# Optimization experiments

Measured on AMD Instinct MI355X. Metric: run time of the kernel, lower is better.

## Reference

```python
import jax, jax.numpy as jnp
import numpy as np
import math

D = 64  # block size == head dim


def _sdpa(q, k, v):
    # q,k,v: [..., n, d]
    d = q.shape[-1]
    scores = jnp.einsum('...nd,...md->...nm', q / math.sqrt(d), k)
    probs = jax.nn.softmax(scores, axis=-1)
    return jnp.einsum('...nm,...md->...nd', probs, v)


def setup_inputs() -> dict:
    key = jax.random.key(0)
    kq, kk, kv = jax.random.split(key, 3)
    B, H, N = 4, 16, 4128  # N = 64*64 + 32 -> nonzero remainder
    q = jax.random.normal(kq, (B, H, N, D), dtype=jnp.float32)
    k = jax.random.normal(kk, (B, H, N, D), dtype=jnp.float32)
    v = jax.random.normal(kv, (B, H, N, D), dtype=jnp.float32)
    return {'q': q, 'k': k, 'v': v}


def reference(q, k, v):
    B, H, N, d = q.shape
    ND = d * (N // d)          # length covered by full DxD blocks
    h = H * (ND // d)          # total number of block-heads
    Q = q[:, :, :ND, :].reshape(B, h, d, d)
    K = k[:, :, :ND, :].reshape(B, h, d, d)
    V = v[:, :, :ND, :].reshape(B, h, d, d)
    attn_main = _sdpa(Q, K, V).reshape(B, H, ND, d)
    attn_rem = _sdpa(q[:, :, ND:, :], k[:, :, ND:, :], v[:, :, ND:, :])
    return jnp.concatenate([attn_main, attn_rem], axis=-2)
```

## Files before the change

kernel.cpp:

```cpp
#include <hip/hip_runtime.h>
#include <math.h>

#define STR 65

__global__ __launch_bounds__(256, 3) void bda_kernel(
    const float* __restrict__ qg,
    const float* __restrict__ kg,
    const float* __restrict__ vg,
    float* __restrict__ og,
    int N, int nblk, int rem) {
  __shared__ float Qs[64 * STR];
  __shared__ float Ks[64 * STR];
  __shared__ float Vs[64 * STR];

  const int wg  = blockIdx.x;
  const int blk = wg % nblk;
  const int bh  = wg / nblk;
  const int nrows = (blk == nblk - 1 && rem != 0) ? rem : 64;
  const size_t base = ((size_t)bh * (size_t)N + (size_t)blk * 64) * 64;

  const int t = threadIdx.x;

#pragma unroll
  for (int i = 0; i < 4; ++i) {
    const int e   = (t << 2) + (i << 10);
    const int row = e >> 6;
    const int col = e & 63;
    float4 qv = make_float4(0.f, 0.f, 0.f, 0.f);
    float4 kv = qv, vv = qv;
    if (row < nrows) {
      qv = *(const float4*)(qg + base + e);
      kv = *(const float4*)(kg + base + e);
      vv = *(const float4*)(vg + base + e);
    }
    const int a = row * STR + col;
    Qs[a + 0] = qv.x; Qs[a + 1] = qv.y; Qs[a + 2] = qv.z; Qs[a + 3] = qv.w;
    Ks[a + 0] = kv.x; Ks[a + 1] = kv.y; Ks[a + 2] = kv.z; Ks[a + 3] = kv.w;
    Vs[a + 0] = vv.x; Vs[a + 1] = vv.y; Vs[a + 2] = vv.z; Vs[a + 3] = vv.w;
  }
  __syncthreads();

  const int tx = t & 15;
  const int ty = t >> 4;
  const int r0 = ty << 2;
  const int c0 = tx << 2;

  float acc[4][4] = {{0.f}};
  {
    const float* q0 = &Qs[(r0 + 0) * STR];
    const float* q1 = &Qs[(r0 + 1) * STR];
    const float* q2 = &Qs[(r0 + 2) * STR];
    const float* q3 = &Qs[(r0 + 3) * STR];
    const float* k0 = &Ks[(c0 + 0) * STR];
    const float* k1 = &Ks[(c0 + 1) * STR];
    const float* k2 = &Ks[(c0 + 2) * STR];
    const float* k3 = &Ks[(c0 + 3) * STR];
#pragma unroll 4
    for (int kk = 0; kk < 64; ++kk) {
      const float a0 = q0[kk], a1 = q1[kk], a2 = q2[kk], a3 = q3[kk];
      const float b0 = k0[kk], b1 = k1[kk], b2 = k2[kk], b3 = k3[kk];
      acc[0][0] += a0 * b0; acc[0][1] += a0 * b1; acc[0][2] += a0 * b2; acc[0][3] += a0 * b3;
      acc[1][0] += a1 * b0; acc[1][1] += a1 * b1; acc[1][2] += a1 * b2; acc[1][3] += a1 * b3;
      acc[2][0] += a2 * b0; acc[2][1] += a2 * b1; acc[2][2] += a2 * b2; acc[2][3] += a2 * b3;
      acc[3][0] += a3 * b0; acc[3][1] += a3 * b1; acc[3][2] += a3 * b2; acc[3][3] += a3 * b3;
    }
  }
  __syncthreads();
#pragma unroll
  for (int i = 0; i < 4; ++i)
#pragma unroll
    for (int j = 0; j < 4; ++j)
      Qs[(r0 + i) * STR + c0 + j] = acc[i][j] * 0.125f;
  __syncthreads();

  {
    const int r = t >> 2;
    const int p = t & 3;
    float s[16];
    float m = -INFINITY;
#pragma unroll
    for (int c = 0; c < 16; ++c) {
      const int col = (p << 4) + c;
      const float x = Qs[r * STR + col];
      s[c] = x;
      m = (col < nrows) ? fmaxf(m, x) : m;
    }
    m = fmaxf(m, __shfl_xor(m, 1));
    m = fmaxf(m, __shfl_xor(m, 2));
    float l = 0.f;
#pragma unroll
    for (int c = 0; c < 16; ++c) {
      const int col = (p << 4) + c;
      const float pv = (col < nrows) ? __expf(s[c] - m) : 0.f;
      s[c] = pv;
      l += pv;
    }
    l += __shfl_xor(l, 1);
    l += __shfl_xor(l, 2);
    const float inv = 1.f / l;
#pragma unroll
    for (int c = 0; c < 16; ++c)
      Qs[r * STR + (p << 4) + c] = s[c] * inv;
  }
  __syncthreads();

  float o[4][4] = {{0.f}};
  {
    const float* p0 = &Qs[(r0 + 0) * STR];
    const float* p1 = &Qs[(r0 + 1) * STR];
    const float* p2 = &Qs[(r0 + 2) * STR];
    const float* p3 = &Qs[(r0 + 3) * STR];
#pragma unroll 4
    for (int j = 0; j < 64; ++j) {
      const float a0 = p0[j], a1 = p1[j], a2 = p2[j], a3 = p3[j];
      const float* vr = &Vs[j * STR + c0];
      const float b0 = vr[0], b1 = vr[1], b2 = vr[2], b3 = vr[3];
      o[0][0] += a0 * b0; o[0][1] += a0 * b1; o[0][2] += a0 * b2; o[0][3] += a0 * b3;
      o[1][0] += a1 * b0; o[1][1] += a1 * b1; o[1][2] += a1 * b2; o[1][3] += a1 * b3;
      o[2][0] += a2 * b0; o[2][1] += a2 * b1; o[2][2] += a2 * b2; o[2][3] += a2 * b3;
      o[3][0] += a3 * b0; o[3][1] += a3 * b1; o[3][2] += a3 * b2; o[3][3] += a3 * b3;
    }
  }
#pragma unroll
  for (int i = 0; i < 4; ++i) {
    const int row = r0 + i;
    if (row < nrows) {
      *(float4*)(og + base + row * 64 + c0) =
          make_float4(o[i][0], o[i][1], o[i][2], o[i][3]);
    }
  }
}

extern "C" void kernel_launch(void* const* d_in, const int* in_sizes, int n_in,
                              void* d_out, int out_size, void* d_ws, size_t ws_size,
                              hipStream_t stream) {
  const float* q = (const float*)d_in[0];
  const float* k = (const float*)d_in[1];
  const float* v = (const float*)d_in[2];
  float* o = (float*)d_out;

  const int N    = 4128;
  const int BH   = in_sizes[0] / (N * 64);
  const int nblk = (N + 63) / 64;
  const int rem  = N & 63;

  bda_kernel<<<dim3(BH * nblk), dim3(256), 0, stream>>>(q, k, v, o, N, nblk, rem);
}
```

Measured before the change: 248.7 us.

## Compute both attention matmuls with split-bf16 MFMA instead of FP32 FMA

Replaces the scalar FP32 outer-product loops for QK^T and PV with MFMA 16x16x32 bf16 instructions. Each operand is split into a high and a low bf16 part, and three products are summed to keep close to FP32 accuracy. Softmax now runs directly on the MFMA accumulator fragments using cross-lane shuffles, and V is staged in registers and later transposed into shared memory. Shared memory drops to four bf16 buffers, which allows a higher occupancy hint. The trade-offs are more conversion work, some loss of precision compared with exact FP32, and output stores that are no longer vectorized.

Result: faster. 219.4 us (-11.8%).

```diff
diff --git a/kernel.cpp b/kernel.cpp
--- a/kernel.cpp
+++ b/kernel.cpp
@@ -1,17 +1,31 @@
 #include <hip/hip_runtime.h>
 #include <math.h>
 
-#define STR 65
+#define STRH 72
 
-__global__ __launch_bounds__(256, 3) void bda_kernel(
+typedef __attribute__((ext_vector_type(8))) short short8;
+typedef __attribute__((ext_vector_type(4))) float f32x4;
+typedef __attribute__((ext_vector_type(4))) short short4v;
+
+__device__ __forceinline__ void split2(float x, unsigned short& h, unsigned short& l) {
+  unsigned u = __float_as_uint(x);
+  unsigned hb = (u + 0x7FFFu + ((u >> 16) & 1u)) & 0xFFFF0000u;
+  h = (unsigned short)(hb >> 16);
+  float r = x - __uint_as_float(hb);
+  unsigned v = __float_as_uint(r);
+  l = (unsigned short)((v + 0x7FFFu + ((v >> 16) & 1u)) >> 16);
+}
+
+__global__ __launch_bounds__(256, 4) void bda_kernel(
     const float* __restrict__ qg,
     const float* __restrict__ kg,
     const float* __restrict__ vg,
     float* __restrict__ og,
     int N, int nblk, int rem) {
-  __shared__ float Qs[64 * STR];
-  __shared__ float Ks[64 * STR];
-  __shared__ float Vs[64 * STR];
+  __shared__ unsigned short Ah[64 * STRH];
+  __shared__ unsigned short Al[64 * STRH];
+  __shared__ unsigned short Bh[64 * STRH];
+  __shared__ unsigned short Bl[64 * STRH];
 
   const int wg  = blockIdx.x;
   const int blk = wg % nblk;
@@ -19,114 +33,144 @@
   const int nrows = (blk == nblk - 1 && rem != 0) ? rem : 64;
   const size_t base = ((size_t)bh * (size_t)N + (size_t)blk * 64) * 64;
 
-  const int t = threadIdx.x;
+  const int t    = threadIdx.x;
+  const int lane = t & 63;
+  const int w    = t >> 6;
 
 #pragma unroll
-  for (int i = 0; i < 4; ++i) {
-    const int e   = (t << 2) + (i << 10);
-    const int row = e >> 6;
-    const int col = e & 63;
+  for (int rnd = 0; rnd < 4; ++rnd) {
+    const int e = (t << 2) + (rnd << 10);
+    const int row = e >> 6, col = e & 63;
     float4 qv = make_float4(0.f, 0.f, 0.f, 0.f);
-    float4 kv = qv, vv = qv;
+    float4 kv = qv;
     if (row < nrows) {
       qv = *(const float4*)(qg + base + e);
       kv = *(const float4*)(kg + base + e);
-      vv = *(const float4*)(vg + base + e);
     }
-    const int a = row * STR + col;
-    Qs[a + 0] = qv.x; Qs[a + 1] = qv.y; Qs[a + 2] = qv.z; Qs[a + 3] = qv.w;
-    Ks[a + 0] = kv.x; Ks[a + 1] = kv.y; Ks[a + 2] = kv.z; Ks[a + 3] = kv.w;
-    Vs[a + 0] = vv.x; Vs[a + 1] = vv.y; Vs[a + 2] = vv.z; Vs[a + 3] = vv.w;
+    unsigned short qh[4], ql[4], kh[4], kl[4];
+    split2(qv.x, qh[0], ql[0]); split2(qv.y, qh[1], ql[1]);
+    split2(qv.z, qh[2], ql[2]); split2(qv.w, qh[3], ql[3]);
+    split2(kv.x, kh[0], kl[0]); split2(kv.y, kh[1], kl[1]);
+    split2(kv.z, kh[2], kl[2]); split2(kv.w, kh[3], kl[3]);
+    const int a = row * STRH + col;
+    *(short4v*)&Ah[a] = (short4v){(short)qh[0], (short)qh[1], (short)qh[2], (short)qh[3]};
+    *(short4v*)&Al[a] = (short4v){(short)ql[0], (short)ql[1], (short)ql[2], (short)ql[3]};
+    *(short4v*)&Bh[a] = (short4v){(short)kh[0], (short)kh[1], (short)kh[2], (short)kh[3]};
+    *(short4v*)&Bl[a] = (short4v){(short)kl[0], (short)kl[1], (short)kl[2], (short)kl[3]};
+  }
+
+  const int vd  = t & 63;
+  const int vkb = (t >> 6) * 16;
+  float vr[16];
+#pragma unroll
+  for (int i = 0; i < 16; ++i) {
+    const int k = vkb + i;
+    vr[i] = (k < nrows) ? vg[base + (size_t)k * 64 + vd] : 0.f;
+  }
+
+  __syncthreads();
+
+  const int colb = lane & 15;
+  const int kofs = (lane >> 4) * 8;
+  const int arow = 16 * w + colb;
+
+  f32x4 acc[4];
+#pragma unroll
+  for (int i = 0; i < 4; ++i) acc[i] = (f32x4){0.f, 0.f, 0.f, 0.f};
+
+#pragma unroll
+  for (int ks = 0; ks < 2; ++ks) {
+    const int kb = ks * 32 + kofs;
+    const short8 ah = *(const short8*)&Ah[arow * STRH + kb];
+    const short8 al = *(const short8*)&Al[arow * STRH + kb];
+#pragma unroll
+    for (int nt = 0; nt < 4; ++nt) {
+      const int brow = 16 * nt + colb;
+      const short8 bhv = *(const short8*)&Bh[brow * STRH + kb];
+      const short8 blv = *(const short8*)&Bl[brow * STRH + kb];
+      acc[nt] = __builtin_amdgcn_mfma_f32_16x16x32_bf16(al, bhv, acc[nt], 0, 0, 0);
+      acc[nt] = __builtin_amdgcn_mfma_f32_16x16x32_bf16(ah, blv, acc[nt], 0, 0, 0);
+      acc[nt] = __builtin_amdgcn_mfma_f32_16x16x32_bf16(ah, bhv, acc[nt], 0, 0, 0);
+    }
+  }
+
+  const int rquad = (lane >> 4) * 4;
+#pragma unroll
+  for (int r = 0; r < 4; ++r) {
+    const int grow = 16 * w + rquad + r;
+    float s[4];
+#pragma unroll
+    for (int nt = 0; nt < 4; ++nt) {
+      const int col = 16 * nt + colb;
+      s[nt] = (col < nrows) ? acc[nt][r] * 0.125f : -1e30f;
+    }
+    float m = fmaxf(fmaxf(s[0], s[1]), fmaxf(s[2], s[3]));
+    m = fmaxf(m, __shfl_xor(m, 1));
+    m = fmaxf(m, __shfl_xor(m, 2));
+    m = fmaxf(m, __shfl_xor(m, 4));
+    m = fmaxf(m, __shfl_xor(m, 8));
+    float p[4];
+    float lsum = 0.f;
+#pragma unroll
+    for (int nt = 0; nt < 4; ++nt) {
+      p[nt] = __expf(s[nt] - m);
+      lsum += p[nt];
+    }
+    lsum += __shfl_xor(lsum, 1);
+    lsum += __shfl_xor(lsum, 2);
+    lsum += __shfl_xor(lsum, 4);
+    lsum += __shfl_xor(lsum, 8);
+    const float inv = 1.f / lsum;
+#pragma unroll
+    for (int nt = 0; nt < 4; ++nt) {
+      unsigned short hh, ll;
+      split2(p[nt] * inv, hh, ll);
+      Ah[grow * STRH + 16 * nt + colb] = hh;
+      Al[grow * STRH + 16 * nt + colb] = ll;
+    }
+  }
+
+  __syncthreads();
+
+#pragma unroll
+  for (int c = 0; c < 4; ++c) {
+    unsigned short h4[4], l4[4];
+#pragma unroll
+    for (int i = 0; i < 4; ++i) split2(vr[4 * c + i], h4[i], l4[i]);
+    const int a = vd * STRH + vkb + 4 * c;
+    *(short4v*)&Bh[a] = (short4v){(short)h4[0], (short)h4[1], (short)h4[2], (short)h4[3]};
+    *(short4v*)&Bl[a] = (short4v){(short)l4[0], (short)l4[1], (short)l4[2], (short)l4[3]};
   }
   __syncthreads();
 
-  const int tx = t & 15;
-  const int ty = t >> 4;
-  const int r0 = ty << 2;
-  const int c0 = tx << 2;
+  f32x4 oacc[4];
+#pragma unroll
+  for (int i = 0; i < 4; ++i) oacc[i] = (f32x4){0.f, 0.f, 0.f, 0.f};
 
-  float acc[4][4] = {{0.f}};
-  {
-    const float* q0 = &Qs[(r0 + 0) * STR];
-    const float* q1 = &Qs[(r0 + 1) * STR];
-    const float* q2 = &Qs[(r0 + 2) * STR];
-    const float* q3 = &Qs[(r0 + 3) * STR];
-    const float* k0 = &Ks[(c0 + 0) * STR];
-    const float* k1 = &Ks[(c0 + 1) * STR];
-    const float* k2 = &Ks[(c0 + 2) * STR];
-    const float* k3 = &Ks[(c0 + 3) * STR];
-#pragma unroll 4
-    for (int kk = 0; kk < 64; ++kk) {
-      const float a0 = q0[kk], a1 = q1[kk], a2 = q2[kk], a3 = q3[kk];
-      const float b0 = k0[kk], b1 = k1[kk], b2 = k2[kk], b3 = k3[kk];
-      acc[0][0] += a0 * b0; acc[0][1] += a0 * b1; acc[0][2] += a0 * b2; acc[0][3] += a0 * b3;
-      acc[1][0] += a1 * b0; acc[1][1] += a1 * b1; acc[1][2] += a1 * b2; acc[1][3] += a1 * b3;
-      acc[2][0] += a2 * b0; acc[2][1] += a2 * b1; acc[2][2] += a2 * b2; acc[2][3] += a2 * b3;
-      acc[3][0] += a3 * b0; acc[3][1] += a3 * b1; acc[3][2] += a3 * b2; acc[3][3] += a3 * b3;
+#pragma unroll
+  for (int ks = 0; ks < 2; ++ks) {
+    const int kb = ks * 32 + kofs;
+    const short8 ph = *(const short8*)&Ah[arow * STRH + kb];
+    const short8 pl = *(const short8*)&Al[arow * STRH + kb];
+#pragma unroll
+    for (int nt = 0; nt < 4; ++nt) {
+      const int vrow = 16 * nt + colb;
+      const short8 vh = *(const short8*)&Bh[vrow * STRH + kb];
+      const short8 vl = *(const short8*)&Bl[vrow * STRH + kb];
+      oacc[nt] = __builtin_amdgcn_mfma_f32_16x16x32_bf16(pl, vh, oacc[nt], 0, 0, 0);
+      oacc[nt] = __builtin_amdgcn_mfma_f32_16x16x32_bf16(ph, vl, oacc[nt], 0, 0, 0);
+      oacc[nt] = __builtin_amdgcn_mfma_f32_16x16x32_bf16(ph, vh, oacc[nt], 0, 0, 0);
     }
   }
-  __syncthreads();
+
 #pragma unroll
-  for (int i = 0; i < 4; ++i)
+  for (int nt = 0; nt < 4; ++nt) {
 #pragma unroll
-    for (int j = 0; j < 4; ++j)
-      Qs[(r0 + i) * STR + c0 + j] = acc[i][j] * 0.125f;
-  __syncthreads();
-
-  {
-    const int r = t >> 2;
-    const int p = t & 3;
-    float s[16];
-    float m = -INFINITY;
-#pragma unroll
-    for (int c = 0; c < 16; ++c) {
-      const int col = (p << 4) + c;
-      const float x = Qs[r * STR + col];
-      s[c] = x;
-      m = (col < nrows) ? fmaxf(m, x) : m;
-    }
-    m = fmaxf(m, __shfl_xor(m, 1));
-    m = fmaxf(m, __shfl_xor(m, 2));
-    float l = 0.f;
-#pragma unroll
-    for (int c = 0; c < 16; ++c) {
-      const int col = (p << 4) + c;
-      const float pv = (col < nrows) ? __expf(s[c] - m) : 0.f;
-      s[c] = pv;
-      l += pv;
-    }
-    l += __shfl_xor(l, 1);
-    l += __shfl_xor(l, 2);
-    const float inv = 1.f / l;
-#pragma unroll
-    for (int c = 0; c < 16; ++c)
-      Qs[r * STR + (p << 4) + c] = s[c] * inv;
-  }
-  __syncthreads();
-
-  float o[4][4] = {{0.f}};
-  {
-    const float* p0 = &Qs[(r0 + 0) * STR];
-    const float* p1 = &Qs[(r0 + 1) * STR];
-    const float* p2 = &Qs[(r0 + 2) * STR];
-    const float* p3 = &Qs[(r0 + 3) * STR];
-#pragma unroll 4
-    for (int j = 0; j < 64; ++j) {
-      const float a0 = p0[j], a1 = p1[j], a2 = p2[j], a3 = p3[j];
-      const float* vr = &Vs[j * STR + c0];
-      const float b0 = vr[0], b1 = vr[1], b2 = vr[2], b3 = vr[3];
-      o[0][0] += a0 * b0; o[0][1] += a0 * b1; o[0][2] += a0 * b2; o[0][3] += a0 * b3;
-      o[1][0] += a1 * b0; o[1][1] += a1 * b1; o[1][2] += a1 * b2; o[1][3] += a1 * b3;
-      o[2][0] += a2 * b0; o[2][1] += a2 * b1; o[2][2] += a2 * b2; o[2][3] += a2 * b3;
-      o[3][0] += a3 * b0; o[3][1] += a3 * b1; o[3][2] += a3 * b2; o[3][3] += a3 * b3;
-    }
-  }
-#pragma unroll
-  for (int i = 0; i < 4; ++i) {
-    const int row = r0 + i;
-    if (row < nrows) {
-      *(float4*)(og + base + row * 64 + c0) =
-          make_float4(o[i][0], o[i][1], o[i][2], o[i][3]);
+    for (int r = 0; r < 4; ++r) {
+      const int row = 16 * w + rquad + r;
+      if (row < nrows) {
+        og[base + (size_t)row * 64 + 16 * nt + colb] = oacc[nt][r];
+      }
     }
   }
 }
```
